# Kernel optimization log

Hardware: AMD Instinct MI355X
Metric: run time of the kernel (lower is better)

Reference implementation:

```python
import jax, jax.numpy as jnp
import numpy as np

B, H, S, D = 2, 16, 2048, 64  # depth = dmodel / num_heads
DMODEL = H * D


def setup_inputs() -> dict:
    key = jax.random.key(0)
    kq, kk, kv, kw = jax.random.split(key, 4)
    Q = jax.random.normal(kq, (B, H, S, D), dtype=jnp.float32)
    K = jax.random.normal(kk, (B, H, S, D), dtype=jnp.float32)
    V = jax.random.normal(kv, (B, H, S, D), dtype=jnp.float32)
    W = jax.random.normal(kw, (DMODEL, DMODEL), dtype=jnp.float32) * (1.0 / np.sqrt(DMODEL))
    b = jnp.zeros((DMODEL,), dtype=jnp.float32)
    return {"Q": Q, "K": K, "V": V, "W": W, "b": b}


def reference(Q, K, V, W, b):
    depth = Q.shape[-1]
    # scores: (B, H, S, S) -- full score matrix, matching the original math
    scores = jnp.einsum('bhqd,bhkd->bhqk', Q, K) / jnp.sqrt(jnp.float32(depth))
    attn = jax.nn.softmax(scores, axis=-1)
    vals = jnp.einsum('bhqk,bhkd->bhqd', attn, V)          # (B, H, S, D)
    vals = jnp.transpose(vals, (0, 2, 1, 3))               # (B, S, H, D)
    concat = vals.reshape(vals.shape[0], vals.shape[1], -1)  # (B, S, dmodel)
    return concat @ W + b
```

## Files before the change

### kernel.cpp

```cpp
#include <hip/hip_runtime.h>
#include <hip/hip_bf16.h>


typedef float  f32x16 __attribute__((ext_vector_type(16)));
typedef float  f32x4v __attribute__((ext_vector_type(4)));
typedef float  f32x2v __attribute__((ext_vector_type(2)));
typedef __bf16 bf16x8 __attribute__((ext_vector_type(8)));
typedef __bf16 bf16x4 __attribute__((ext_vector_type(4)));
typedef __bf16 bf16x2 __attribute__((ext_vector_type(2)));

static constexpr int Bn = 2, Hn = 16, Sn = 2048, Dn = 64, DM = 1024;
static constexpr size_t QKV_ELEMS = (size_t)Bn * Hn * Sn * Dn;

#define QSCALE 0.18033688011112042f

#if __has_builtin(__builtin_amdgcn_cvt_pk_bf16_f32)
static __device__ __forceinline__ unsigned pack2(float a, float b) {
  bf16x2 t = __builtin_amdgcn_cvt_pk_bf16_f32(a, b);
  union { bf16x2 v; unsigned u; } c; c.v = t; return c.u;
}
#else
static __device__ __forceinline__ unsigned pack2(float a, float b) {
  union { __bf16 h; unsigned short s; } ua, ub;
  ua.h = (__bf16)a; ub.h = (__bf16)b;
  return (unsigned)ua.s | ((unsigned)ub.s << 16);
}
#endif

static __device__ __forceinline__ void unzip8(const unsigned* wds, bf16x8* r0, bf16x8* r1) {
  union { unsigned u[4]; bf16x8 v; } a, b;
#pragma unroll
  for (int i = 0; i < 4; ++i) {
    unsigned lo = wds[2 * i], hi = wds[2 * i + 1];
    a.u[i] = (lo & 0xffffu) | (hi << 16);
    b.u[i] = (lo >> 16) | (hi & 0xffff0000u);
  }
  *r0 = a.v; *r1 = b.v;
}

__global__ __launch_bounds__(256) void convert_all(
    const float* __restrict__ q, const float* __restrict__ k,
    const float* __restrict__ v, const float* __restrict__ w,
    __bf16* __restrict__ qo, __bf16* __restrict__ ko,
    __bf16* __restrict__ vt, __bf16* __restrict__ wt) {
  __shared__ __bf16 T[64][74];
  const int bid = blockIdx.x, t = threadIdx.x;

  if (bid < 4096) {
    const int z = bid >> 11;
    const int bx = bid & 2047;
    const float* src = z ? k : q;
    __bf16* dst      = z ? ko : qo;
    const float scale = z ? 1.0f : QSCALE;
    size_t i = ((size_t)bx * 256 + t) * 8;
    f32x4v a = *(const f32x4v*)(src + i);
    f32x4v b = *(const f32x4v*)(src + i + 4);
    bf16x8 o;
#pragma unroll
    for (int j = 0; j < 4; ++j) { o[j] = (__bf16)(a[j] * scale); o[4 + j] = (__bf16)(b[j] * scale); }
    *(bf16x8*)(dst + i) = o;
    return;
  }

  const float* s0;
  __bf16* dst0;
  size_t dst_stride;
  {
    const int r = t >> 2, c0 = (t & 3) * 16;
    if (bid < 5120) {
      const int idx = bid - 4096;
      const int kv0 = (idx & 31) * 64, bh = idx >> 5;
      s0 = v + ((size_t)bh * Sn + kv0 + r) * Dn + c0;
      dst0 = vt + (size_t)bh * Dn * Sn + kv0;
      dst_stride = Sn;
    } else {
      const int idx = bid - 5120;
      const int nt = (idx & 15) * 64, kt = (idx >> 4) * 64;
      s0 = w + (size_t)(kt + r) * DM + nt + c0;
      dst0 = wt + (size_t)nt * DM + kt;
      dst_stride = DM;
    }
    union { bf16x8 v8; unsigned u[4]; } o0, o1;
#pragma unroll
    for (int i = 0; i < 2; ++i) {
      f32x4v f = *(const f32x4v*)(s0 + i * 4);
#pragma unroll
      for (int j = 0; j < 4; ++j) o0.v8[i * 4 + j] = (__bf16)f[j];
    }
#pragma unroll
    for (int i = 0; i < 2; ++i) {
      f32x4v f = *(const f32x4v*)(s0 + 8 + i * 4);
#pragma unroll
      for (int j = 0; j < 4; ++j) o1.v8[i * 4 + j] = (__bf16)f[j];
    }
#pragma unroll
    for (int j = 0; j < 4; ++j) {
      *(unsigned*)&T[r][c0 + 2 * j]     = o0.u[j];
      *(unsigned*)&T[r][c0 + 8 + 2 * j] = o1.u[j];
    }
  }
  __syncthreads();
  const int rp = t >> 3, k0 = (t & 7) * 8;
  unsigned wds[8];
#pragma unroll
  for (int i = 0; i < 8; ++i) wds[i] = *(const unsigned*)&T[k0 + i][2 * rp];
  bf16x8 r0, r1; unzip8(wds, &r0, &r1);
  __bf16* d0 = dst0 + (size_t)(2 * rp) * dst_stride + k0;
  *(bf16x8*)d0 = r0;
  *(bf16x8*)(d0 + dst_stride) = r1;
}

__global__ __launch_bounds__(256, 3) void attn(
    const __bf16* __restrict__ Qb, const __bf16* __restrict__ Kb,
    const __bf16* __restrict__ Vtg, __bf16* __restrict__ Cc) {
  const int tid = threadIdx.x;
  const int wave = tid >> 6, lane = tid & 63;
  const int ln = lane & 31, g = lane >> 5;
  const int qg = wave >> 1, kh = wave & 1;
  const int qb = blockIdx.x, h = blockIdx.y, bz = blockIdx.z;

  __shared__ __bf16 smem[2][2][64][72];
  __bf16 (*Ks)[64][72] = smem[0];
  __bf16 (*Vs)[64][72] = smem[1];

  const size_t hoff = (size_t)(bz * Hn + h) * Sn * Dn;
  const __bf16* Qp = Qb + hoff + (size_t)(qb * 128 + qg * 64) * Dn;
  const __bf16* Kp = Kb + hoff;
  const __bf16* Vp = Vtg + hoff;

  bf16x8 qf[2][4];
#pragma unroll
  for (int qt = 0; qt < 2; ++qt)
#pragma unroll
    for (int ks = 0; ks < 4; ++ks)
      qf[qt][ks] = *(const bf16x8*)(Qp + (size_t)(qt * 32 + ln) * Dn + ks * 16 + g * 8);

  const int sr = tid >> 2, sc = (tid & 3) * 16;
  const __bf16* kbase = Kp + (size_t)sr * Dn + sc;
  const __bf16* vbase = Vp + (size_t)sr * Sn + sc;

  bf16x8 k0r = *(const bf16x8*)kbase, k1r = *(const bf16x8*)(kbase + 8);
  bf16x8 v0r = *(const bf16x8*)vbase, v1r = *(const bf16x8*)(vbase + 8);
  *(bf16x8*)&Ks[0][sr][sc]     = k0r;
  *(bf16x8*)&Ks[0][sr][sc + 8] = k1r;
  *(bf16x8*)&Vs[0][sr][sc]     = v0r;
  *(bf16x8*)&Vs[0][sr][sc + 8] = v1r;
  k0r = *(const bf16x8*)(kbase + (size_t)64 * Dn);
  k1r = *(const bf16x8*)(kbase + (size_t)64 * Dn + 8);
  v0r = *(const bf16x8*)(vbase + 64);
  v1r = *(const bf16x8*)(vbase + 64 + 8);
  __syncthreads();

  f32x16 O[2][2] = {{{}, {}}, {{}, {}}};
  float Lown[2] = {0.0f, 0.0f};
  constexpr int NT = Sn / 64;

  for (int kt = 0; kt < NT; ++kt) {
    const int buf = kt & 1;

    bf16x8 kf[4];
#pragma unroll
    for (int ks = 0; ks < 4; ++ks)
      kf[ks] = *(const bf16x8*)&Ks[buf][kh * 32 + ln][ks * 16 + g * 8];

    unsigned w[2][8];
#pragma unroll
    for (int qt = 0; qt < 2; ++qt) {
      f32x16 s = {};
#pragma unroll
      for (int ks = 0; ks < 4; ++ks)
        s = __builtin_amdgcn_mfma_f32_32x32x16_bf16(kf[ks], qf[qt][ks], s, 0, 0, 0);
      float p[16];
#pragma unroll
      for (int r = 0; r < 16; ++r) p[r] = __builtin_amdgcn_exp2f(s[r]);
      f32x2v s2 = {0.0f, 0.0f};
#pragma unroll
      for (int tt = 0; tt < 8; ++tt) { f32x2v t2 = {p[2 * tt], p[2 * tt + 1]}; s2 += t2; }
      Lown[qt] += s2[0] + s2[1];
#pragma unroll
      for (int tt = 0; tt < 8; ++tt) w[qt][tt] = pack2(p[2 * tt], p[2 * tt + 1]);
    }

    if (kt + 1 < NT) {
      const int nb = buf ^ 1;
      *(bf16x8*)&Ks[nb][sr][sc]     = k0r;
      *(bf16x8*)&Ks[nb][sr][sc + 8] = k1r;
      *(bf16x8*)&Vs[nb][sr][sc]     = v0r;
      *(bf16x8*)&Vs[nb][sr][sc + 8] = v1r;
      if (kt + 2 < NT) {
        const __bf16* kp = kbase + (size_t)(kt + 2) * 64 * Dn;
        k0r = *(const bf16x8*)kp; k1r = *(const bf16x8*)(kp + 8);
        const __bf16* vp = vbase + (kt + 2) * 64;
        v0r = *(const bf16x8*)vp; v1r = *(const bf16x8*)(vp + 8);
      }
    }

#pragma unroll
    for (int s4 = 0; s4 < 2; ++s4) {
      const int cb = kh * 32 + s4 * 16 + g * 4;
      union { bf16x4 h[2]; bf16x8 v; } vf0, vf1;
      vf0.h[0] = *(const bf16x4*)&Vs[buf][ln][cb];
      vf0.h[1] = *(const bf16x4*)&Vs[buf][ln][cb + 8];
      vf1.h[0] = *(const bf16x4*)&Vs[buf][32 + ln][cb];
      vf1.h[1] = *(const bf16x4*)&Vs[buf][32 + ln][cb + 8];
#pragma unroll
      for (int qt = 0; qt < 2; ++qt) {
        union { unsigned u[4]; bf16x8 v; } pu;
        pu.u[0] = w[qt][s4 * 4 + 0];
        pu.u[1] = w[qt][s4 * 4 + 1];
        pu.u[2] = w[qt][s4 * 4 + 2];
        pu.u[3] = w[qt][s4 * 4 + 3];
        O[qt][0] = __builtin_amdgcn_mfma_f32_32x32x16_bf16(vf0.v, pu.v, O[qt][0], 0, 0, 0);
        O[qt][1] = __builtin_amdgcn_mfma_f32_32x32x16_bf16(vf1.v, pu.v, O[qt][1], 0, 0, 0);
      }
    }
    __syncthreads();
  }

  float Lred[2];
#pragma unroll
  for (int qt = 0; qt < 2; ++qt) Lred[qt] = Lown[qt] + __shfl_xor(Lown[qt], 32);

  float* Ex = (float*)smem;
  const int slot = (qg * 64 + lane) * 68;
  if (kh == 1) {
#pragma unroll
    for (int qt = 0; qt < 2; ++qt)
#pragma unroll
      for (int dh = 0; dh < 2; ++dh)
#pragma unroll
        for (int i = 0; i < 4; ++i) {
          f32x4v t = {O[qt][dh][4 * i], O[qt][dh][4 * i + 1],
                      O[qt][dh][4 * i + 2], O[qt][dh][4 * i + 3]};
          *(f32x4v*)&Ex[slot + qt * 32 + dh * 16 + 4 * i] = t;
        }
    Ex[slot + 64] = Lred[0];
    Ex[slot + 65] = Lred[1];
  }
  __syncthreads();
  float inv[2] = {0.0f, 0.0f};
  if (kh == 0) {
#pragma unroll
    for (int qt = 0; qt < 2; ++qt)
#pragma unroll
      for (int dh = 0; dh < 2; ++dh)
#pragma unroll
        for (int i = 0; i < 4; ++i) {
          f32x4v t = *(const f32x4v*)&Ex[slot + qt * 32 + dh * 16 + 4 * i];
#pragma unroll
          for (int c = 0; c < 4; ++c) O[qt][dh][4 * i + c] += t[c];
        }
    inv[0] = 1.0f / (Lred[0] + Ex[slot + 64]);
    inv[1] = 1.0f / (Lred[1] + Ex[slot + 65]);
  }
  __syncthreads();
  __bf16* T = (__bf16*)smem;
  if (kh == 0) {
#pragma unroll
    for (int qt = 0; qt < 2; ++qt)
#pragma unroll
      for (int dh = 0; dh < 2; ++dh)
#pragma unroll
        for (int a = 0; a < 4; ++a) {
          bf16x4 t4;
#pragma unroll
          for (int c = 0; c < 4; ++c) t4[c] = (__bf16)(O[qt][dh][4 * a + c] * inv[qt]);
          *(bf16x4*)&T[(qg * 64 + qt * 32 + ln) * 72 + dh * 32 + 8 * a + 4 * g] = t4;
        }
  }
  __syncthreads();
  const int q0 = qb * 128;
#pragma unroll
  for (int i = 0; i < 4; ++i) {
    const int rq = i * 32 + (tid >> 3);
    const int c8 = (tid & 7) * 8;
    bf16x8 o = *(const bf16x8*)&T[rq * 72 + c8];
    size_t base = (((size_t)bz * Sn + q0 + rq) * Hn + h) * Dn + c8;
    *(bf16x8*)&Cc[base] = o;
  }
}

__global__ __launch_bounds__(256, 2) void proj(
    const __bf16* __restrict__ A, const __bf16* __restrict__ Wt,
    const float* __restrict__ bias, float* __restrict__ out) {
  const int tid = threadIdx.x, wave = tid >> 6, lane = tid & 63;
  const int ln = lane & 31, g = lane >> 5;
  const int bm = blockIdx.x, bn = blockIdx.y;
  __shared__ __bf16 As[2][128][72];
  __shared__ __bf16 Bs[2][64][72];
  const int ar = tid >> 1, ac = (tid & 1) * 32;
  const int br = tid >> 2, bc = (tid & 3) * 16;
  f32x16 acc0 = {}, acc1 = {};
  const __bf16* Ap = A + (size_t)(bm * 128) * DM;
  const __bf16* Wp = Wt + (size_t)(bn * 64) * DM;

  bf16x8 a0, a1, a2, a3, b0, b1;
  {
    const __bf16* ap = Ap + (size_t)ar * DM + ac;
    a0 = *(const bf16x8*)ap;        a1 = *(const bf16x8*)(ap + 8);
    a2 = *(const bf16x8*)(ap + 16); a3 = *(const bf16x8*)(ap + 24);
    const __bf16* wp = Wp + (size_t)br * DM + bc;
    b0 = *(const bf16x8*)wp; b1 = *(const bf16x8*)(wp + 8);
  }
  *(bf16x8*)&As[0][ar][ac]      = a0;
  *(bf16x8*)&As[0][ar][ac + 8]  = a1;
  *(bf16x8*)&As[0][ar][ac + 16] = a2;
  *(bf16x8*)&As[0][ar][ac + 24] = a3;
  *(bf16x8*)&Bs[0][br][bc]      = b0;
  *(bf16x8*)&Bs[0][br][bc + 8]  = b1;
  {
    const __bf16* ap = Ap + (size_t)ar * DM + 64 + ac;
    a0 = *(const bf16x8*)ap;        a1 = *(const bf16x8*)(ap + 8);
    a2 = *(const bf16x8*)(ap + 16); a3 = *(const bf16x8*)(ap + 24);
    const __bf16* wp = Wp + (size_t)br * DM + 64 + bc;
    b0 = *(const bf16x8*)wp; b1 = *(const bf16x8*)(wp + 8);
  }
  __syncthreads();

  constexpr int KT = DM / 64;
  for (int kt = 0; kt < KT; ++kt) {
    const int buf = kt & 1;
#pragma unroll
    for (int ks = 0; ks < 4; ++ks) {
      bf16x8 af  = *(const bf16x8*)&As[buf][wave * 32 + ln][ks * 16 + g * 8];
      bf16x8 wf0 = *(const bf16x8*)&Bs[buf][ln][ks * 16 + g * 8];
      bf16x8 wf1 = *(const bf16x8*)&Bs[buf][32 + ln][ks * 16 + g * 8];
      acc0 = __builtin_amdgcn_mfma_f32_32x32x16_bf16(af, wf0, acc0, 0, 0, 0);
      acc1 = __builtin_amdgcn_mfma_f32_32x32x16_bf16(af, wf1, acc1, 0, 0, 0);
    }
    if (kt + 1 < KT) {
      const int nb = buf ^ 1;
      *(bf16x8*)&As[nb][ar][ac]      = a0;
      *(bf16x8*)&As[nb][ar][ac + 8]  = a1;
      *(bf16x8*)&As[nb][ar][ac + 16] = a2;
      *(bf16x8*)&As[nb][ar][ac + 24] = a3;
      *(bf16x8*)&Bs[nb][br][bc]      = b0;
      *(bf16x8*)&Bs[nb][br][bc + 8]  = b1;
      if (kt + 2 < KT) {
        const __bf16* ap = Ap + (size_t)ar * DM + (kt + 2) * 64 + ac;
        a0 = *(const bf16x8*)ap;        a1 = *(const bf16x8*)(ap + 8);
        a2 = *(const bf16x8*)(ap + 16); a3 = *(const bf16x8*)(ap + 24);
        const __bf16* wp = Wp + (size_t)br * DM + (kt + 2) * 64 + bc;
        b0 = *(const bf16x8*)wp; b1 = *(const bf16x8*)(wp + 8);
      }
    }
    __syncthreads();
  }
  float bv0 = bias[bn * 64 + ln], bv1 = bias[bn * 64 + 32 + ln];
#pragma unroll
  for (int r = 0; r < 16; ++r) {
    int row = bm * 128 + wave * 32 + (r & 3) + ((r >> 2) << 3) + (g << 2);
    out[(size_t)row * DM + bn * 64 + ln]      = acc0[r] + bv0;
    out[(size_t)row * DM + bn * 64 + 32 + ln] = acc1[r] + bv1;
  }
}

extern "C" void kernel_launch(void* const* d_in, const int* in_sizes, int n_in,
                              void* d_out, int out_size, void* d_ws, size_t ws_size,
                              hipStream_t stream) {
  const float* Q = (const float*)d_in[0];
  const float* K = (const float*)d_in[1];
  const float* V = (const float*)d_in[2];
  const float* W = (const float*)d_in[3];
  const float* b = (const float*)d_in[4];
  float* out = (float*)d_out;

  __bf16* ws  = (__bf16*)d_ws;
  __bf16* Qb  = ws;
  __bf16* Kb  = Qb + QKV_ELEMS;
  __bf16* Vtg = Kb + QKV_ELEMS;
  __bf16* Cc  = Vtg + QKV_ELEMS;
  __bf16* Wt  = Cc + QKV_ELEMS;

  convert_all<<<dim3(5376, 1, 1), 256, 0, stream>>>(Q, K, V, W, Qb, Kb, Vtg, Wt);
  attn<<<dim3(Sn / 128, Hn, Bn), 256, 0, stream>>>(Qb, Kb, Vtg, Cc);
  proj<<<dim3(Bn * Sn / 128, DM / 64, 1), 256, 0, stream>>>(Cc, Wt, b, out);
}
```

Baseline: 159.2 us.

## Split-K projection with atomics, MFMA row-sums, padded V tile, swizzled proj LDS

The output projection is split along K into two halves. The output is pre-filled with the bias inside the conversion kernel, and the partial sums are added with unsafe atomic adds, which doubles the number of projection blocks. In the attention kernel, the softmax denominator is now computed with an extra MFMA against a vector of ones instead of a scalar sum, and the V shared tile is padded to 76 columns to reduce bank conflicts. The projection LDS moves to an XOR-swizzled layout without padding and raises its occupancy hint. These changes add atomic traffic on the output and make the summation order nondeterministic.

```diff
diff --git a/kernel.cpp b/kernel.cpp
--- a/kernel.cpp
+++ b/kernel.cpp
@@ -4,7 +4,6 @@
 
 typedef float  f32x16 __attribute__((ext_vector_type(16)));
 typedef float  f32x4v __attribute__((ext_vector_type(4)));
-typedef float  f32x2v __attribute__((ext_vector_type(2)));
 typedef __bf16 bf16x8 __attribute__((ext_vector_type(8)));
 typedef __bf16 bf16x4 __attribute__((ext_vector_type(4)));
 typedef __bf16 bf16x2 __attribute__((ext_vector_type(2)));
@@ -41,10 +40,22 @@
 __global__ __launch_bounds__(256) void convert_all(
     const float* __restrict__ q, const float* __restrict__ k,
     const float* __restrict__ v, const float* __restrict__ w,
+    const float* __restrict__ bias, float* __restrict__ out,
     __bf16* __restrict__ qo, __bf16* __restrict__ ko,
     __bf16* __restrict__ vt, __bf16* __restrict__ wt) {
   __shared__ __bf16 T[64][74];
   const int bid = blockIdx.x, t = threadIdx.x;
+
+  if (bid >= 5376) {
+    const int idx = bid - 5376;
+    size_t base = (size_t)idx * 2048 + (size_t)t * 8;
+    const int col = (int)(base & 1023);
+    f32x4v b0 = *(const f32x4v*)(bias + col);
+    f32x4v b1 = *(const f32x4v*)(bias + col + 4);
+    *(f32x4v*)(out + base) = b0;
+    *(f32x4v*)(out + base + 4) = b1;
+    return;
+  }
 
   if (bid < 4096) {
     const int z = bid >> 11;
@@ -119,9 +130,9 @@
   const int qg = wave >> 1, kh = wave & 1;
   const int qb = blockIdx.x, h = blockIdx.y, bz = blockIdx.z;
 
-  __shared__ __bf16 smem[2][2][64][72];
-  __bf16 (*Ks)[64][72] = smem[0];
-  __bf16 (*Vs)[64][72] = smem[1];
+  __shared__ char pool[2 * 64 * 72 * 2 + 2 * 64 * 76 * 2];
+  __bf16 (*Ks)[64][72] = (__bf16(*)[64][72])pool;
+  __bf16 (*Vs)[64][76] = (__bf16(*)[64][76])(pool + 2 * 64 * 72 * 2);
 
   const size_t hoff = (size_t)(bz * Hn + h) * Sn * Dn;
   const __bf16* Qp = Qb + hoff + (size_t)(qb * 128 + qg * 64) * Dn;
@@ -135,16 +146,25 @@
     for (int ks = 0; ks < 4; ++ks)
       qf[qt][ks] = *(const bf16x8*)(Qp + (size_t)(qt * 32 + ln) * Dn + ks * 16 + g * 8);
 
+  bf16x8 ones;
+#pragma unroll
+  for (int i = 0; i < 8; ++i) ones[i] = (__bf16)1.0f;
+
   const int sr = tid >> 2, sc = (tid & 3) * 16;
   const __bf16* kbase = Kp + (size_t)sr * Dn + sc;
   const __bf16* vbase = Vp + (size_t)sr * Sn + sc;
 
   bf16x8 k0r = *(const bf16x8*)kbase, k1r = *(const bf16x8*)(kbase + 8);
   bf16x8 v0r = *(const bf16x8*)vbase, v1r = *(const bf16x8*)(vbase + 8);
-  *(bf16x8*)&Ks[0][sr][sc]     = k0r;
-  *(bf16x8*)&Ks[0][sr][sc + 8] = k1r;
-  *(bf16x8*)&Vs[0][sr][sc]     = v0r;
-  *(bf16x8*)&Vs[0][sr][sc + 8] = v1r;
+  {
+    *(bf16x8*)&Ks[0][sr][sc]     = k0r;
+    *(bf16x8*)&Ks[0][sr][sc + 8] = k1r;
+    union { bf16x8 v; bf16x4 h[2]; } u0, u1; u0.v = v0r; u1.v = v1r;
+    *(bf16x4*)&Vs[0][sr][sc]      = u0.h[0];
+    *(bf16x4*)&Vs[0][sr][sc + 4]  = u0.h[1];
+    *(bf16x4*)&Vs[0][sr][sc + 8]  = u1.h[0];
+    *(bf16x4*)&Vs[0][sr][sc + 12] = u1.h[1];
+  }
   k0r = *(const bf16x8*)(kbase + (size_t)64 * Dn);
   k1r = *(const bf16x8*)(kbase + (size_t)64 * Dn + 8);
   v0r = *(const bf16x8*)(vbase + 64);
@@ -152,7 +172,7 @@
   __syncthreads();
 
   f32x16 O[2][2] = {{{}, {}}, {{}, {}}};
-  float Lown[2] = {0.0f, 0.0f};
+  f32x16 Ls[2] = {{}, {}};
   constexpr int NT = Sn / 64;
 
   for (int kt = 0; kt < NT; ++kt) {
@@ -173,10 +193,6 @@
       float p[16];
 #pragma unroll
       for (int r = 0; r < 16; ++r) p[r] = __builtin_amdgcn_exp2f(s[r]);
-      f32x2v s2 = {0.0f, 0.0f};
-#pragma unroll
-      for (int tt = 0; tt < 8; ++tt) { f32x2v t2 = {p[2 * tt], p[2 * tt + 1]}; s2 += t2; }
-      Lown[qt] += s2[0] + s2[1];
 #pragma unroll
       for (int tt = 0; tt < 8; ++tt) w[qt][tt] = pack2(p[2 * tt], p[2 * tt + 1]);
     }
@@ -185,8 +201,11 @@
       const int nb = buf ^ 1;
       *(bf16x8*)&Ks[nb][sr][sc]     = k0r;
       *(bf16x8*)&Ks[nb][sr][sc + 8] = k1r;
-      *(bf16x8*)&Vs[nb][sr][sc]     = v0r;
-      *(bf16x8*)&Vs[nb][sr][sc + 8] = v1r;
+      union { bf16x8 v; bf16x4 h[2]; } u0, u1; u0.v = v0r; u1.v = v1r;
+      *(bf16x4*)&Vs[nb][sr][sc]      = u0.h[0];
+      *(bf16x4*)&Vs[nb][sr][sc + 4]  = u0.h[1];
+      *(bf16x4*)&Vs[nb][sr][sc + 8]  = u1.h[0];
+      *(bf16x4*)&Vs[nb][sr][sc + 12] = u1.h[1];
       if (kt + 2 < NT) {
         const __bf16* kp = kbase + (size_t)(kt + 2) * 64 * Dn;
         k0r = *(const bf16x8*)kp; k1r = *(const bf16x8*)(kp + 8);
@@ -212,16 +231,13 @@
         pu.u[3] = w[qt][s4 * 4 + 3];
         O[qt][0] = __builtin_amdgcn_mfma_f32_32x32x16_bf16(vf0.v, pu.v, O[qt][0], 0, 0, 0);
         O[qt][1] = __builtin_amdgcn_mfma_f32_32x32x16_bf16(vf1.v, pu.v, O[qt][1], 0, 0, 0);
+        Ls[qt]   = __builtin_amdgcn_mfma_f32_32x32x16_bf16(ones,  pu.v, Ls[qt],   0, 0, 0);
       }
     }
     __syncthreads();
   }
 
-  float Lred[2];
-#pragma unroll
-  for (int qt = 0; qt < 2; ++qt) Lred[qt] = Lown[qt] + __shfl_xor(Lown[qt], 32);
-
-  float* Ex = (float*)smem;
+  float* Ex = (float*)pool;
   const int slot = (qg * 64 + lane) * 68;
   if (kh == 1) {
 #pragma unroll
@@ -234,8 +250,8 @@
                       O[qt][dh][4 * i + 2], O[qt][dh][4 * i + 3]};
           *(f32x4v*)&Ex[slot + qt * 32 + dh * 16 + 4 * i] = t;
         }
-    Ex[slot + 64] = Lred[0];
-    Ex[slot + 65] = Lred[1];
+    Ex[slot + 64] = Ls[0][0];
+    Ex[slot + 65] = Ls[1][0];
   }
   __syncthreads();
   float inv[2] = {0.0f, 0.0f};
@@ -250,11 +266,11 @@
 #pragma unroll
           for (int c = 0; c < 4; ++c) O[qt][dh][4 * i + c] += t[c];
         }
-    inv[0] = 1.0f / (Lred[0] + Ex[slot + 64]);
-    inv[1] = 1.0f / (Lred[1] + Ex[slot + 65]);
-  }
-  __syncthreads();
-  __bf16* T = (__bf16*)smem;
+    inv[0] = 1.0f / (Ls[0][0] + Ex[slot + 64]);
+    inv[1] = 1.0f / (Ls[1][0] + Ex[slot + 65]);
+  }
+  __syncthreads();
+  __bf16* T = (__bf16*)pool;
   if (kh == 0) {
 #pragma unroll
     for (int qt = 0; qt < 2; ++qt)
@@ -280,78 +296,89 @@
   }
 }
 
-__global__ __launch_bounds__(256, 2) void proj(
+__global__ __launch_bounds__(256, 3) void proj(
     const __bf16* __restrict__ A, const __bf16* __restrict__ Wt,
-    const float* __restrict__ bias, float* __restrict__ out) {
+    float* __restrict__ out) {
   const int tid = threadIdx.x, wave = tid >> 6, lane = tid & 63;
   const int ln = lane & 31, g = lane >> 5;
-  const int bm = blockIdx.x, bn = blockIdx.y;
-  __shared__ __bf16 As[2][128][72];
-  __shared__ __bf16 Bs[2][64][72];
-  const int ar = tid >> 1, ac = (tid & 1) * 32;
-  const int br = tid >> 2, bc = (tid & 3) * 16;
+  const int bm = blockIdx.x, bn = blockIdx.y, kz = blockIdx.z;
+  const int kbase0 = kz * 512;
+
+  __shared__ __bf16 As[2][128 * 64];
+  __shared__ __bf16 Bs[2][64 * 64];
+
+  const int ra = tid >> 1, ca = (tid & 1) * 4;
+  const int rb = tid >> 2, cbb = (tid & 3) * 2;
   f32x16 acc0 = {}, acc1 = {};
-  const __bf16* Ap = A + (size_t)(bm * 128) * DM;
-  const __bf16* Wp = Wt + (size_t)(bn * 64) * DM;
-
-  bf16x8 a0, a1, a2, a3, b0, b1;
+  const __bf16* Ap = A + (size_t)(bm * 128) * DM + kbase0;
+  const __bf16* Wp = Wt + (size_t)(bn * 64) * DM + kbase0;
+
+  bf16x8 ar0, ar1, ar2, ar3, br0, br1;
   {
-    const __bf16* ap = Ap + (size_t)ar * DM + ac;
-    a0 = *(const bf16x8*)ap;        a1 = *(const bf16x8*)(ap + 8);
-    a2 = *(const bf16x8*)(ap + 16); a3 = *(const bf16x8*)(ap + 24);
-    const __bf16* wp = Wp + (size_t)br * DM + bc;
-    b0 = *(const bf16x8*)wp; b1 = *(const bf16x8*)(wp + 8);
-  }
-  *(bf16x8*)&As[0][ar][ac]      = a0;
-  *(bf16x8*)&As[0][ar][ac + 8]  = a1;
-  *(bf16x8*)&As[0][ar][ac + 16] = a2;
-  *(bf16x8*)&As[0][ar][ac + 24] = a3;
-  *(bf16x8*)&Bs[0][br][bc]      = b0;
-  *(bf16x8*)&Bs[0][br][bc + 8]  = b1;
+    const __bf16* ap = Ap + (size_t)ra * DM + ca * 8;
+    ar0 = *(const bf16x8*)ap;        ar1 = *(const bf16x8*)(ap + 8);
+    ar2 = *(const bf16x8*)(ap + 16); ar3 = *(const bf16x8*)(ap + 24);
+    const __bf16* wp = Wp + (size_t)rb * DM + cbb * 8;
+    br0 = *(const bf16x8*)wp; br1 = *(const bf16x8*)(wp + 8);
+  }
   {
-    const __bf16* ap = Ap + (size_t)ar * DM + 64 + ac;
-    a0 = *(const bf16x8*)ap;        a1 = *(const bf16x8*)(ap + 8);
-    a2 = *(const bf16x8*)(ap + 16); a3 = *(const bf16x8*)(ap + 24);
-    const __bf16* wp = Wp + (size_t)br * DM + 64 + bc;
-    b0 = *(const bf16x8*)wp; b1 = *(const bf16x8*)(wp + 8);
-  }
-  __syncthreads();
-
-  constexpr int KT = DM / 64;
+    const int swa = ra & 7, swb = rb & 7;
+    *(bf16x8*)&As[0][ra * 64 + ((ca + 0) ^ swa) * 8] = ar0;
+    *(bf16x8*)&As[0][ra * 64 + ((ca + 1) ^ swa) * 8] = ar1;
+    *(bf16x8*)&As[0][ra * 64 + ((ca + 2) ^ swa) * 8] = ar2;
+    *(bf16x8*)&As[0][ra * 64 + ((ca + 3) ^ swa) * 8] = ar3;
+    *(bf16x8*)&Bs[0][rb * 64 + ((cbb + 0) ^ swb) * 8] = br0;
+    *(bf16x8*)&Bs[0][rb * 64 + ((cbb + 1) ^ swb) * 8] = br1;
+  }
+  {
+    const __bf16* ap = Ap + (size_t)ra * DM + 64 + ca * 8;
+    ar0 = *(const bf16x8*)ap;        ar1 = *(const bf16x8*)(ap + 8);
+    ar2 = *(const bf16x8*)(ap + 16); ar3 = *(const bf16x8*)(ap + 24);
+    const __bf16* wp = Wp + (size_t)rb * DM + 64 + cbb * 8;
+    br0 = *(const bf16x8*)wp; br1 = *(const bf16x8*)(wp + 8);
+  }
+  __syncthreads();
+
+  constexpr int KT = 512 / 64;
+  const int Ra = wave * 32 + ln, swR = Ra & 7;
+  const int swl = ln & 7;
   for (int kt = 0; kt < KT; ++kt) {
     const int buf = kt & 1;
 #pragma unroll
     for (int ks = 0; ks < 4; ++ks) {
-      bf16x8 af  = *(const bf16x8*)&As[buf][wave * 32 + ln][ks * 16 + g * 8];
-      bf16x8 wf0 = *(const bf16x8*)&Bs[buf][ln][ks * 16 + g * 8];
-      bf16x8 wf1 = *(const bf16x8*)&Bs[buf][32 + ln][ks * 16 + g * 8];
+      const int cidx = ks * 2 + g;
+      bf16x8 af  = *(const bf16x8*)&As[buf][Ra * 64 + (cidx ^ swR) * 8];
+      bf16x8 wf0 = *(const bf16x8*)&Bs[buf][ln * 64 + (cidx ^ swl) * 8];
+      bf16x8 wf1 = *(const bf16x8*)&Bs[buf][(32 + ln) * 64 + (cidx ^ swl) * 8];
       acc0 = __builtin_amdgcn_mfma_f32_32x32x16_bf16(af, wf0, acc0, 0, 0, 0);
       acc1 = __builtin_amdgcn_mfma_f32_32x32x16_bf16(af, wf1, acc1, 0, 0, 0);
     }
     if (kt + 1 < KT) {
       const int nb = buf ^ 1;
-      *(bf16x8*)&As[nb][ar][ac]      = a0;
-      *(bf16x8*)&As[nb][ar][ac + 8]  = a1;
-      *(bf16x8*)&As[nb][ar][ac + 16] = a2;
-      *(bf16x8*)&As[nb][ar][ac + 24] = a3;
-      *(bf16x8*)&Bs[nb][br][bc]      = b0;
-      *(bf16x8*)&Bs[nb][br][bc + 8]  = b1;
+      const int swa = ra & 7, swb = rb & 7;
+      *(bf16x8*)&As[nb][ra * 64 + ((ca + 0) ^ swa) * 8] = ar0;
+      *(bf16x8*)&As[nb][ra * 64 + ((ca + 1) ^ swa) * 8] = ar1;
+      *(bf16x8*)&As[nb][ra * 64 + ((ca + 2) ^ swa) * 8] = ar2;
+      *(bf16x8*)&As[nb][ra * 64 + ((ca + 3) ^ swa) * 8] = ar3;
+      *(bf16x8*)&Bs[nb][rb * 64 + ((cbb + 0) ^ swb) * 8] = br0;
+      *(bf16x8*)&Bs[nb][rb * 64 + ((cbb + 1) ^ swb) * 8] = br1;
       if (kt + 2 < KT) {
-        const __bf16* ap = Ap + (size_t)ar * DM + (kt + 2) * 64 + ac;
-        a0 = *(const bf16x8*)ap;        a1 = *(const bf16x8*)(ap + 8);
-        a2 = *(const bf16x8*)(ap + 16); a3 = *(const bf16x8*)(ap + 24);
-        const __bf16* wp = Wp + (size_t)br * DM + (kt + 2) * 64 + bc;
-        b0 = *(const bf16x8*)wp; b1 = *(const bf16x8*)(wp + 8);
+        const __bf16* ap = Ap + (size_t)ra * DM + (kt + 2) * 64 + ca * 8;
+        ar0 = *(const bf16x8*)ap;        ar1 = *(const bf16x8*)(ap + 8);
+        ar2 = *(const bf16x8*)(ap + 16); ar3 = *(const bf16x8*)(ap + 24);
+        const __bf16* wp = Wp + (size_t)rb * DM + (kt + 2) * 64 + cbb * 8;
+        br0 = *(const bf16x8*)wp; br1 = *(const bf16x8*)(wp + 8);
       }
     }
     __syncthreads();
   }
-  float bv0 = bias[bn * 64 + ln], bv1 = bias[bn * 64 + 32 + ln];
+
 #pragma unroll
   for (int r = 0; r < 16; ++r) {
     int row = bm * 128 + wave * 32 + (r & 3) + ((r >> 2) << 3) + (g << 2);
-    out[(size_t)row * DM + bn * 64 + ln]      = acc0[r] + bv0;
-    out[(size_t)row * DM + bn * 64 + 32 + ln] = acc1[r] + bv1;
+    float* o = out + (size_t)row * DM + bn * 64;
+    unsafeAtomicAdd(o + ln,      acc0[r]);
+    unsafeAtomicAdd(o + 32 + ln, acc1[r]);
   }
 }
 
@@ -372,7 +399,8 @@
   __bf16* Cc  = Vtg + QKV_ELEMS;
   __bf16* Wt  = Cc + QKV_ELEMS;
 
-  convert_all<<<dim3(5376, 1, 1), 256, 0, stream>>>(Q, K, V, W, Qb, Kb, Vtg, Wt);
+  convert_all<<<dim3(7424, 1, 1), 256, 0, stream>>>(Q, K, V, W, b, out,
+                                                    Qb, Kb, Vtg, Wt);
   attn<<<dim3(Sn / 128, Hn, Bn), 256, 0, stream>>>(Qb, Kb, Vtg, Cc);
-  proj<<<dim3(Bn * Sn / 128, DM / 64, 1), 256, 0, stream>>>(Cc, Wt, b, out);
-}
+  proj<<<dim3(Bn * Sn / 128, DM / 64, 2), 256, 0, stream>>>(Cc, Wt, out);
+}
```

Result: slower. 222.0 us (+39.4%).
